# Kernel optimization log

Hardware: AMD Instinct MI355X
Metric: run time of the kernel (lower is better)

Reference implementation:

```python
import jax, jax.numpy as jnp
import numpy as np

N_NODES = 100000
N_EDGES = 1600000
D_IN, D_HID, D_OUT = 512, 256, 32


def setup_inputs() -> dict:
    key = jax.random.key(0)
    ks = jax.random.split(key, 8)
    features = jax.random.normal(ks[0], (N_NODES, D_IN), dtype=jnp.float32)
    A_data = jax.random.uniform(ks[1], (N_EDGES,), dtype=jnp.float32)
    A_row = jax.random.randint(ks[2], (N_EDGES,), 0, N_NODES, dtype=jnp.int32)
    A_col = jax.random.randint(ks[3], (N_EDGES,), 0, N_NODES, dtype=jnp.int32)
    # MLP params (glorot-ish scaling)
    W1 = jax.random.normal(ks[4], (D_IN, D_HID), dtype=jnp.float32) * (1.0 / np.sqrt(D_IN))
    b1 = jnp.zeros((D_HID,), dtype=jnp.float32)
    W2 = jax.random.normal(ks[5], (D_HID, D_OUT), dtype=jnp.float32) * (1.0 / np.sqrt(D_HID))
    b2 = jnp.zeros((D_OUT,), dtype=jnp.float32)
    return {"features": features, "A_data": A_data, "W1": W1, "b1": b1,
            "W2": W2, "b2": b2, "A_row": A_row, "A_col": A_col}


def reference(features, A_data, W1, b1, W2, b2, A_row, A_col):
    # head_transform: 2-layer MLP (is_training=False -> dropout identity)
    h = jax.nn.relu(features @ W1 + b1)          # [N, D_HID]
    X = h @ W2 + b2                              # [N, D_OUT]
    # propagator dropout: rate=0.0 / eval mode -> identity on A
    # sparse COO A @ X: gather columns, scale by edge values, scatter-add to rows
    msgs = A_data[:, None] * X[A_col]            # [E, D_OUT]
    out = jax.ops.segment_sum(msgs, A_row, num_segments=N_NODES)  # [N, D_OUT]
    return out
```

## Files before the change

### kernel.cpp

```cpp
#include <hip/hip_runtime.h>
#include <hip/hip_bf16.h>

typedef __bf16 bf16;
typedef __attribute__((ext_vector_type(8))) __bf16 bf16x8;
typedef __attribute__((ext_vector_type(4))) float f32x4;

constexpr int D_IN  = 512;
constexpr int D_HID = 256;
constexpr int D_OUT = 32;
constexpr int BM = 64;
constexpr int BK = 64;
constexpr int HCP = 40;
constexpr int CAP = 64;
constexpr int NSLICE = 8;

#define GLOBAL_AS(p) ((const __attribute__((address_space(1))) void*)(p))
#define LDS_AS(p)    ((__attribute__((address_space(3))) void*)(p))

__global__ __launch_bounds__(256) void prep_kernel(
    const float* __restrict__ W1, const float* __restrict__ W2,
    bf16* __restrict__ W1T, bf16* __restrict__ W2T)
{
    int idx = blockIdx.x * 256 + threadIdx.x;
    if (idx < D_IN * D_HID) {
        int k = idx / D_HID, n = idx % D_HID;
        W1T[n * D_IN + k] = (bf16)W1[idx];
    }
    int j = idx - D_IN * D_HID;
    if (j >= 0 && j < D_HID * D_OUT) {
        int k = j / D_OUT, n = j % D_OUT;
        W2T[n * D_HID + k] = (bf16)W2[j];
    }
}

__global__ __launch_bounds__(256) void mlp_fill_kernel(
    const float* __restrict__ feat,
    const bf16* __restrict__ W1T, const bf16* __restrict__ W2T,
    const float* __restrict__ b1, const float* __restrict__ b2,
    float* __restrict__ X, int N,
    const int* __restrict__ Arow, const int* __restrict__ Acol,
    const float* __restrict__ Adata, int* __restrict__ cursor,
    int2* __restrict__ pairs, int E, int rps, int mlpB)
{
    if ((int)blockIdx.x >= mlpB) {
        int slice = blockIdx.x & (NSLICE - 1);
        int e = ((blockIdx.x - mlpB) >> 3) * 256 + threadIdx.x;
        if (e >= E) return;
        int r = Arow[e];
        if ((unsigned)(r - slice * rps) >= (unsigned)rps) return;
        int p = atomicAdd(&cursor[r], 1);
        if (p < CAP) {
            int2 pk;
            pk.x = Acol[e];
            pk.y = __float_as_int(Adata[e]);
            pairs[(long)r * CAP + p] = pk;
        }
        return;
    }

    __shared__ __align__(16) char smem[D_HID * BK * sizeof(bf16)];
    bf16* Bsm = (bf16*)smem;
    bf16* Hc  = (bf16*)smem;

    const int tid  = threadIdx.x;
    const int wave = tid >> 6;
    const int lane = tid & 63;
    const int ln   = lane & 15;
    const int q    = lane >> 4;
    const int mw   = wave * 16;
    const int r0   = blockIdx.x * BM;

    const long arow = (long)min(r0 + mw + ln, N - 1);
    const float* asrc = feat + arow * D_IN + q * 8;
    bf16x8 afr[16];
    #pragma unroll
    for (int f = 0; f < 16; ++f) {
        float4 g0 = *(const float4*)(asrc + f * 32);
        float4 g1 = *(const float4*)(asrc + f * 32 + 4);
        bf16x8 v;
        v[0] = (bf16)g0.x; v[1] = (bf16)g0.y; v[2] = (bf16)g0.z; v[3] = (bf16)g0.w;
        v[4] = (bf16)g1.x; v[5] = (bf16)g1.y; v[6] = (bf16)g1.z; v[7] = (bf16)g1.w;
        afr[f] = v;
    }

    f32x4 acc[16] = {};

    #pragma unroll
    for (int s = 0; s < 8; ++s) {
        const int k0 = s * BK;
        #pragma unroll
        for (int i = 0; i < 8; ++i) {
            int c  = i * 256 + wave * 64 + lane;
            int sl = (c & 7) ^ ((c >> 3) & 7);
            const bf16* gsrc = W1T + ((c >> 3) * D_IN + k0 + sl * 8);
            bf16* lbase = Bsm + (i * 256 + wave * 64) * 8;
            __builtin_amdgcn_global_load_lds(GLOBAL_AS(gsrc), LDS_AS(lbase), 16, 0, 0);
        }
        __syncthreads();

        const int psl0 = (0 * 4 + q) ^ (ln & 7);
        #pragma unroll
        for (int t = 0; t < 16; ++t) {
            bf16x8 bfv = *(const bf16x8*)&Bsm[(t * 16 + ln) * BK + psl0 * 8];
            acc[t] = __builtin_amdgcn_mfma_f32_16x16x32_bf16(afr[2 * s], bfv, acc[t], 0, 0, 0);
        }
        const int psl1 = (1 * 4 + q) ^ (ln & 7);
        #pragma unroll
        for (int t = 0; t < 16; ++t) {
            bf16x8 bfv = *(const bf16x8*)&Bsm[(t * 16 + ln) * BK + psl1 * 8];
            acc[t] = __builtin_amdgcn_mfma_f32_16x16x32_bf16(afr[2 * s + 1], bfv, acc[t], 0, 0, 0);
        }
        __syncthreads();
    }

    f32x4 acc2[2] = {};
    #pragma unroll
    for (int cc = 0; cc < 8; ++cc) {
        #pragma unroll
        for (int tt = 0; tt < 2; ++tt) {
            int t = cc * 2 + tt;
            float bb = b1[t * 16 + ln];
            #pragma unroll
            for (int i = 0; i < 4; ++i) {
                int row = mw + q * 4 + i;
                float v = acc[t][i] + bb;
                Hc[row * HCP + tt * 16 + ln] = (bf16)fmaxf(v, 0.0f);
            }
        }
        __syncthreads();
        bf16x8 af2 = *(const bf16x8*)&Hc[(mw + ln) * HCP + q * 8];
        int kg = cc * 32 + q * 8;
        #pragma unroll
        for (int t2 = 0; t2 < 2; ++t2) {
            bf16x8 bfv = *(const bf16x8*)&W2T[(t2 * 16 + ln) * D_HID + kg];
            acc2[t2] = __builtin_amdgcn_mfma_f32_16x16x32_bf16(af2, bfv, acc2[t2], 0, 0, 0);
        }
        __syncthreads();
    }

    #pragma unroll
    for (int t = 0; t < 2; ++t) {
        int c = t * 16 + ln;
        float bb = b2[c];
        #pragma unroll
        for (int i = 0; i < 4; ++i) {
            int row = r0 + mw + q * 4 + i;
            if (row < N) X[row * D_OUT + c] = acc2[t][i] + bb;
        }
    }
}

__global__ __launch_bounds__(256) void reduce_kernel(
    const int* __restrict__ cursor, const int2* __restrict__ pairs,
    const float* __restrict__ X, float* __restrict__ out, int N)
{
    int w    = threadIdx.x >> 6;
    int lane = threadIdx.x & 63;
    int r    = blockIdx.x * 4 + w;
    if (r >= N) return;
    int slot = lane >> 3;
    int dg   = lane & 7;
    int deg  = min(cursor[r], CAP);
    long off = (long)r * CAP;
    f32x4 acc = {0.0f, 0.0f, 0.0f, 0.0f};
    for (int i = slot; i < deg; i += 8) {
        int2  pk = pairs[off + i];
        float a  = __int_as_float(pk.y);
        f32x4 x  = *(const f32x4*)(X + (long)pk.x * D_OUT + dg * 4);
        acc += a * x;
    }
    #pragma unroll
    for (int d = 8; d < 64; d <<= 1) {
        acc[0] += __shfl_xor(acc[0], d, 64);
        acc[1] += __shfl_xor(acc[1], d, 64);
        acc[2] += __shfl_xor(acc[2], d, 64);
        acc[3] += __shfl_xor(acc[3], d, 64);
    }
    if (slot == 0) *(f32x4*)(out + (long)r * D_OUT + dg * 4) = acc;
}

__global__ __launch_bounds__(256) void scatter_kernel(
    const float* __restrict__ Adata, const int* __restrict__ Arow,
    const int* __restrict__ Acol, const float* __restrict__ X,
    float* __restrict__ out, int E)
{
    int idx = blockIdx.x * 256 + threadIdx.x;
    int e = idx >> 3;
    int g = idx & 7;
    if (e >= E) return;
    int   col = Acol[e];
    int   row = Arow[e];
    float a   = Adata[e];
    float4 x = *(const float4*)(X + (long)col * D_OUT + g * 4);
    float* o = out + (long)row * D_OUT + g * 4;
    unsafeAtomicAdd(o + 0, a * x.x);
    unsafeAtomicAdd(o + 1, a * x.y);
    unsafeAtomicAdd(o + 2, a * x.z);
    unsafeAtomicAdd(o + 3, a * x.w);
}

extern "C" void kernel_launch(void* const* d_in, const int* in_sizes, int n_in,
                              void* d_out, int out_size, void* d_ws, size_t ws_size,
                              hipStream_t stream)
{
    const float* feat  = (const float*)d_in[0];
    const float* Adata = (const float*)d_in[1];
    const float* W1    = (const float*)d_in[2];
    const float* b1    = (const float*)d_in[3];
    const float* W2    = (const float*)d_in[4];
    const float* b2    = (const float*)d_in[5];
    const int*   Arow  = (const int*)d_in[6];
    const int*   Acol  = (const int*)d_in[7];

    const int N = in_sizes[0] / D_IN;
    const int E = in_sizes[1];

    char* p = (char*)d_ws;
    auto alloc = [&](size_t bytes) {
        char* q = p;
        p += (bytes + 255) & ~(size_t)255;
        return q;
    };
    float* X      = (float*)alloc((size_t)N * D_OUT * sizeof(float));
    bf16*  W1T    = (bf16*) alloc((size_t)D_IN * D_HID * sizeof(bf16));
    bf16*  W2T    = (bf16*) alloc((size_t)D_HID * D_OUT * sizeof(bf16));
    int*   cursor = (int*)  alloc((size_t)N * sizeof(int));
    int2*  pairs  = (int2*) alloc((size_t)N * CAP * sizeof(int2));
    size_t need = (size_t)(p - (char*)d_ws);
    const bool use_bucket = (need <= ws_size);

    float* out = (float*)d_out;

    int prep_elems = D_IN * D_HID + D_HID * D_OUT;
    prep_kernel<<<(prep_elems + 255) / 256, 256, 0, stream>>>(W1, W2, W1T, W2T);

    int mlpB = (N + BM - 1) / BM;

    if (use_bucket) {
        hipMemsetAsync(cursor, 0, (size_t)N * sizeof(int), stream);
        int rps   = (N + NSLICE - 1) / NSLICE;
        int fillB = NSLICE * ((E + 255) / 256);
        mlp_fill_kernel<<<mlpB + fillB, 256, 0, stream>>>(
            feat, W1T, W2T, b1, b2, X, N,
            Arow, Acol, Adata, cursor, pairs, E, rps, mlpB);
        reduce_kernel<<<(N + 3) / 4, 256, 0, stream>>>(cursor, pairs, X, out, N);
    } else {
        mlp_fill_kernel<<<mlpB, 256, 0, stream>>>(
            feat, W1T, W2T, b1, b2, X, N,
            Arow, Acol, Adata, nullptr, nullptr, E, 1, mlpB);
        hipMemsetAsync(out, 0, (size_t)out_size * sizeof(float), stream);
        long scatter_threads = (long)E * 8;
        scatter_kernel<<<(scatter_threads + 255) / 256, 256, 0, stream>>>(
            Adata, Arow, Acol, X, out, E);
    }
}
```

Before: 588.1 us.

## Replace row-bucket fill and reduce with row-sliced atomic scatter

Drops the per-row bucket scheme (atomic cursor fill into fixed-capacity pair slots, then a per-row gather reduce) and the MLP-side fusion of the fill. Edges are now scattered straight into the output with float atomics from a persistent grid; each block handles one of eight row slices so its atomic targets stay within a smaller L2-resident window. The MLP kernel also stops preloading all A fragments into registers and loads them per K step, which lowers register pressure but exposes more load latency. The change removes the extra pair buffer write/read and the capacity truncation, at the cost of many contended atomics and every slice re-reading the full edge row array.

```diff
diff --git a/kernel.cpp b/kernel.cpp
--- a/kernel.cpp
+++ b/kernel.cpp
@@ -11,8 +11,8 @@
 constexpr int BM = 64;
 constexpr int BK = 64;
 constexpr int HCP = 40;
-constexpr int CAP = 64;
 constexpr int NSLICE = 8;
+constexpr int SCHB = 2048;
 
 #define GLOBAL_AS(p) ((const __attribute__((address_space(1))) void*)(p))
 #define LDS_AS(p)    ((__attribute__((address_space(3))) void*)(p))
@@ -33,31 +33,12 @@
     }
 }
 
-__global__ __launch_bounds__(256) void mlp_fill_kernel(
+__global__ __launch_bounds__(256) void fused_mlp_kernel(
     const float* __restrict__ feat,
     const bf16* __restrict__ W1T, const bf16* __restrict__ W2T,
     const float* __restrict__ b1, const float* __restrict__ b2,
-    float* __restrict__ X, int N,
-    const int* __restrict__ Arow, const int* __restrict__ Acol,
-    const float* __restrict__ Adata, int* __restrict__ cursor,
-    int2* __restrict__ pairs, int E, int rps, int mlpB)
-{
-    if ((int)blockIdx.x >= mlpB) {
-        int slice = blockIdx.x & (NSLICE - 1);
-        int e = ((blockIdx.x - mlpB) >> 3) * 256 + threadIdx.x;
-        if (e >= E) return;
-        int r = Arow[e];
-        if ((unsigned)(r - slice * rps) >= (unsigned)rps) return;
-        int p = atomicAdd(&cursor[r], 1);
-        if (p < CAP) {
-            int2 pk;
-            pk.x = Acol[e];
-            pk.y = __float_as_int(Adata[e]);
-            pairs[(long)r * CAP + p] = pk;
-        }
-        return;
-    }
-
+    float* __restrict__ X, int N)
+{
     __shared__ __align__(16) char smem[D_HID * BK * sizeof(bf16)];
     bf16* Bsm = (bf16*)smem;
     bf16* Hc  = (bf16*)smem;
@@ -70,24 +51,12 @@
     const int mw   = wave * 16;
     const int r0   = blockIdx.x * BM;
 
+    f32x4 acc[16] = {};
+
     const long arow = (long)min(r0 + mw + ln, N - 1);
     const float* asrc = feat + arow * D_IN + q * 8;
-    bf16x8 afr[16];
-    #pragma unroll
-    for (int f = 0; f < 16; ++f) {
-        float4 g0 = *(const float4*)(asrc + f * 32);
-        float4 g1 = *(const float4*)(asrc + f * 32 + 4);
-        bf16x8 v;
-        v[0] = (bf16)g0.x; v[1] = (bf16)g0.y; v[2] = (bf16)g0.z; v[3] = (bf16)g0.w;
-        v[4] = (bf16)g1.x; v[5] = (bf16)g1.y; v[6] = (bf16)g1.z; v[7] = (bf16)g1.w;
-        afr[f] = v;
-    }
-
-    f32x4 acc[16] = {};
-
-    #pragma unroll
-    for (int s = 0; s < 8; ++s) {
-        const int k0 = s * BK;
+
+    for (int k0 = 0; k0 < D_IN; k0 += BK) {
         #pragma unroll
         for (int i = 0; i < 8; ++i) {
             int c  = i * 256 + wave * 64 + lane;
@@ -96,19 +65,34 @@
             bf16* lbase = Bsm + (i * 256 + wave * 64) * 8;
             __builtin_amdgcn_global_load_lds(GLOBAL_AS(gsrc), LDS_AS(lbase), 16, 0, 0);
         }
-        __syncthreads();
-
-        const int psl0 = (0 * 4 + q) ^ (ln & 7);
-        #pragma unroll
-        for (int t = 0; t < 16; ++t) {
-            bf16x8 bfv = *(const bf16x8*)&Bsm[(t * 16 + ln) * BK + psl0 * 8];
-            acc[t] = __builtin_amdgcn_mfma_f32_16x16x32_bf16(afr[2 * s], bfv, acc[t], 0, 0, 0);
-        }
-        const int psl1 = (1 * 4 + q) ^ (ln & 7);
-        #pragma unroll
-        for (int t = 0; t < 16; ++t) {
-            bf16x8 bfv = *(const bf16x8*)&Bsm[(t * 16 + ln) * BK + psl1 * 8];
-            acc[t] = __builtin_amdgcn_mfma_f32_16x16x32_bf16(afr[2 * s + 1], bfv, acc[t], 0, 0, 0);
+
+        bf16x8 af0, af1;
+        {
+            float4 f0 = *(const float4*)(asrc + k0);
+            float4 f1 = *(const float4*)(asrc + k0 + 4);
+            af0[0] = (bf16)f0.x; af0[1] = (bf16)f0.y; af0[2] = (bf16)f0.z; af0[3] = (bf16)f0.w;
+            af0[4] = (bf16)f1.x; af0[5] = (bf16)f1.y; af0[6] = (bf16)f1.z; af0[7] = (bf16)f1.w;
+            float4 f2 = *(const float4*)(asrc + k0 + 32);
+            float4 f3 = *(const float4*)(asrc + k0 + 36);
+            af1[0] = (bf16)f2.x; af1[1] = (bf16)f2.y; af1[2] = (bf16)f2.z; af1[3] = (bf16)f2.w;
+            af1[4] = (bf16)f3.x; af1[5] = (bf16)f3.y; af1[6] = (bf16)f3.z; af1[7] = (bf16)f3.w;
+        }
+
+        __syncthreads();
+
+        {
+            const int psl0 = (0 * 4 + q) ^ (ln & 7);
+            #pragma unroll
+            for (int t = 0; t < 16; ++t) {
+                bf16x8 bfv = *(const bf16x8*)&Bsm[(t * 16 + ln) * BK + psl0 * 8];
+                acc[t] = __builtin_amdgcn_mfma_f32_16x16x32_bf16(af0, bfv, acc[t], 0, 0, 0);
+            }
+            const int psl1 = (1 * 4 + q) ^ (ln & 7);
+            #pragma unroll
+            for (int t = 0; t < 16; ++t) {
+                bf16x8 bfv = *(const bf16x8*)&Bsm[(t * 16 + ln) * BK + psl1 * 8];
+                acc[t] = __builtin_amdgcn_mfma_f32_16x16x32_bf16(af1, bfv, acc[t], 0, 0, 0);
+            }
         }
         __syncthreads();
     }
@@ -150,53 +134,31 @@
     }
 }
 
-__global__ __launch_bounds__(256) void reduce_kernel(
-    const int* __restrict__ cursor, const int2* __restrict__ pairs,
-    const float* __restrict__ X, float* __restrict__ out, int N)
-{
-    int w    = threadIdx.x >> 6;
-    int lane = threadIdx.x & 63;
-    int r    = blockIdx.x * 4 + w;
-    if (r >= N) return;
-    int slot = lane >> 3;
-    int dg   = lane & 7;
-    int deg  = min(cursor[r], CAP);
-    long off = (long)r * CAP;
-    f32x4 acc = {0.0f, 0.0f, 0.0f, 0.0f};
-    for (int i = slot; i < deg; i += 8) {
-        int2  pk = pairs[off + i];
-        float a  = __int_as_float(pk.y);
-        f32x4 x  = *(const f32x4*)(X + (long)pk.x * D_OUT + dg * 4);
-        acc += a * x;
-    }
-    #pragma unroll
-    for (int d = 8; d < 64; d <<= 1) {
-        acc[0] += __shfl_xor(acc[0], d, 64);
-        acc[1] += __shfl_xor(acc[1], d, 64);
-        acc[2] += __shfl_xor(acc[2], d, 64);
-        acc[3] += __shfl_xor(acc[3], d, 64);
-    }
-    if (slot == 0) *(f32x4*)(out + (long)r * D_OUT + dg * 4) = acc;
-}
-
 __global__ __launch_bounds__(256) void scatter_kernel(
-    const float* __restrict__ Adata, const int* __restrict__ Arow,
-    const int* __restrict__ Acol, const float* __restrict__ X,
-    float* __restrict__ out, int E)
-{
-    int idx = blockIdx.x * 256 + threadIdx.x;
-    int e = idx >> 3;
-    int g = idx & 7;
-    if (e >= E) return;
-    int   col = Acol[e];
-    int   row = Arow[e];
-    float a   = Adata[e];
-    float4 x = *(const float4*)(X + (long)col * D_OUT + g * 4);
-    float* o = out + (long)row * D_OUT + g * 4;
-    unsafeAtomicAdd(o + 0, a * x.x);
-    unsafeAtomicAdd(o + 1, a * x.y);
-    unsafeAtomicAdd(o + 2, a * x.z);
-    unsafeAtomicAdd(o + 3, a * x.w);
+    const int* __restrict__ Arow, const int* __restrict__ Acol,
+    const float* __restrict__ Adata, const float* __restrict__ X,
+    float* __restrict__ out, int E, int rps)
+{
+    int slice = blockIdx.x & (NSLICE - 1);
+    int esub  = threadIdx.x >> 3;
+    int dg    = threadIdx.x & 7;
+    int nch = (E + 31) / 32;
+    for (int ch = blockIdx.x >> 3; ch < nch; ch += SCHB) {
+        int e = ch * 32 + esub;
+        if (e < E) {
+            int r = Arow[e];
+            if ((unsigned)(r - slice * rps) < (unsigned)rps) {
+                float a   = Adata[e];
+                int   col = Acol[e];
+                f32x4 x = *(const f32x4*)(X + (long)col * D_OUT + dg * 4);
+                float* o = out + (long)r * D_OUT + dg * 4;
+                unsafeAtomicAdd(o + 0, a * x[0]);
+                unsafeAtomicAdd(o + 1, a * x[1]);
+                unsafeAtomicAdd(o + 2, a * x[2]);
+                unsafeAtomicAdd(o + 3, a * x[3]);
+            }
+        }
+    }
 }
 
 extern "C" void kernel_launch(void* const* d_in, const int* in_sizes, int n_in,
@@ -221,36 +183,21 @@
         p += (bytes + 255) & ~(size_t)255;
         return q;
     };
-    float* X      = (float*)alloc((size_t)N * D_OUT * sizeof(float));
-    bf16*  W1T    = (bf16*) alloc((size_t)D_IN * D_HID * sizeof(bf16));
-    bf16*  W2T    = (bf16*) alloc((size_t)D_HID * D_OUT * sizeof(bf16));
-    int*   cursor = (int*)  alloc((size_t)N * sizeof(int));
-    int2*  pairs  = (int2*) alloc((size_t)N * CAP * sizeof(int2));
-    size_t need = (size_t)(p - (char*)d_ws);
-    const bool use_bucket = (need <= ws_size);
+    float* X   = (float*)alloc((size_t)N * D_OUT * sizeof(float));
+    bf16*  W1T = (bf16*) alloc((size_t)D_IN * D_HID * sizeof(bf16));
+    bf16*  W2T = (bf16*) alloc((size_t)D_HID * D_OUT * sizeof(bf16));
+    (void)ws_size;
 
     float* out = (float*)d_out;
 
     int prep_elems = D_IN * D_HID + D_HID * D_OUT;
     prep_kernel<<<(prep_elems + 255) / 256, 256, 0, stream>>>(W1, W2, W1T, W2T);
 
-    int mlpB = (N + BM - 1) / BM;
-
-    if (use_bucket) {
-        hipMemsetAsync(cursor, 0, (size_t)N * sizeof(int), stream);
-        int rps   = (N + NSLICE - 1) / NSLICE;
-        int fillB = NSLICE * ((E + 255) / 256);
-        mlp_fill_kernel<<<mlpB + fillB, 256, 0, stream>>>(
-            feat, W1T, W2T, b1, b2, X, N,
-            Arow, Acol, Adata, cursor, pairs, E, rps, mlpB);
-        reduce_kernel<<<(N + 3) / 4, 256, 0, stream>>>(cursor, pairs, X, out, N);
-    } else {
-        mlp_fill_kernel<<<mlpB, 256, 0, stream>>>(
-            feat, W1T, W2T, b1, b2, X, N,
-            Arow, Acol, Adata, nullptr, nullptr, E, 1, mlpB);
-        hipMemsetAsync(out, 0, (size_t)out_size * sizeof(float), stream);
-        long scatter_threads = (long)E * 8;
-        scatter_kernel<<<(scatter_threads + 255) / 256, 256, 0, stream>>>(
-            Adata, Arow, Acol, X, out, E);
-    }
-}
+    fused_mlp_kernel<<<(N + BM - 1) / BM, 256, 0, stream>>>(
+        feat, W1T, W2T, b1, b2, X, N);
+
+    hipMemsetAsync(out, 0, (size_t)out_size * sizeof(float), stream);
+    int rps = (N + NSLICE - 1) / NSLICE;
+    scatter_kernel<<<NSLICE * SCHB, 256, 0, stream>>>(
+        Arow, Acol, Adata, X, out, E, rps);
+}
```

New measurement: 0.9997 ms. 70.0% more time.
